# Kernel optimization log

Measured on AMD Instinct MI355X. Metric: run time of the kernel, lower is better.

The kernel has to match this reference:

```python
import math
import jax, jax.numpy as jnp
import numpy as np

H = 16  # head_count

def setup_inputs() -> dict:
    key = jax.random.key(0)
    ks = jax.random.split(key, 7)
    B, S, D = 2, 2048, 1024
    query = jax.random.normal(ks[0], (B, S, D), dtype=jnp.float32)
    # mask: True = masked position (matches masked_fill_ semantics)
    mask = jax.random.randint(ks[1], (B, S, S), 0, 2) > 0
    scale = 1.0 / math.sqrt(D)  # xavier-ish init scale
    Wq = jax.random.normal(ks[2], (D, D), dtype=jnp.float32) * scale
    Wk = jax.random.normal(ks[3], (D, D), dtype=jnp.float32) * scale
    Wv = jax.random.normal(ks[4], (D, D), dtype=jnp.float32) * scale
    Wo = jax.random.normal(ks[5], (D, D), dtype=jnp.float32) * scale
    bo = jnp.zeros((D,), dtype=jnp.float32)
    return {"query": query, "mask": mask, "Wq": Wq, "Wk": Wk, "Wv": Wv, "Wo": Wo, "bo": bo}


def reference(query, mask, Wq, Wk, Wv, Wo, bo):
    B, S, D = query.shape
    dh = D // H

    def split_heads(x):  # [B,S,D] -> [B,H,S,dh]
        return x.reshape(B, S, H, dh).transpose(0, 2, 1, 3)

    # torch nn.Linear computes x @ W.T (bias-free for q/k/v)
    q = split_heads(query @ Wq.T) * (1.0 / math.sqrt(dh))
    k = split_heads(query @ Wk.T)
    v = split_heads(query @ Wv.T)

    scores = jnp.einsum('bhqd,bhkd->bhqk', q, k)           # [B,H,S,S]
    scores = jnp.where(mask[:, None, :, :], jnp.float32(-1e18), scores)
    weights = jax.nn.softmax(scores, axis=-1)               # dropout=0 -> identity
    ctx = jnp.einsum('bhqk,bhkd->bhqd', weights, v)         # [B,H,S,dh]
    ctx = ctx.transpose(0, 2, 1, 3).reshape(B, S, D)        # combine heads
    return ctx @ Wo.T + bo
```

## Files before the change

### kernel.cpp

```cpp
#include <hip/hip_runtime.h>

#define S_LEN 2048
#define D_MODEL 1024
#define NH 16
#define DH 64

typedef __bf16 bf16x8 __attribute__((ext_vector_type(8)));
typedef __bf16 bf16x4 __attribute__((ext_vector_type(4)));
typedef float f32x4 __attribute__((ext_vector_type(4)));

__device__ __forceinline__ unsigned short f2bf(float f) {
  unsigned int x = __float_as_uint(f);
  x += 0x7fffu + ((x >> 16) & 1u);
  return (unsigned short)(x >> 16);
}

__device__ __forceinline__ bf16x4 cvt4(f32x4 v) {
  return __builtin_convertvector(v, bf16x4);
}

__device__ __forceinline__ float exp2raw(float x) {
#if __has_builtin(__builtin_amdgcn_exp2f)
  return __builtin_amdgcn_exp2f(x);
#else
  return exp2f(x);
#endif
}

__device__ __forceinline__ f32x4 mfma16(bf16x8 a, bf16x8 b, f32x4 c) {
  return __builtin_amdgcn_mfma_f32_16x16x32_bf16(a, b, c, 0, 0, 0);
}

__device__ __forceinline__ void gl2lds(const unsigned short* g, unsigned short* l) {
  __builtin_amdgcn_global_load_lds(
      (__attribute__((address_space(1))) void*)g,
      (__attribute__((address_space(3))) void*)l, 16, 0, 0);
}

__global__ __launch_bounds__(256) void prep_kernel(
    const float* __restrict__ q, const float* __restrict__ wq,
    const float* __restrict__ wk, const float* __restrict__ wv,
    const float* __restrict__ wo, const int* __restrict__ mask,
    unsigned short* __restrict__ qbf, unsigned short* __restrict__ wbf,
    unsigned long long* __restrict__ bits) {
  const int bx = blockIdx.x;
  if (bx < 32768) {
    int i = bx * 256 + threadIdx.x;
    unsigned long long bal = __ballot(mask[i] != 0);
    if ((threadIdx.x & 63) == 0) bits[i >> 6] = bal;
  } else {
    const long t = (long)(bx - 32768) * 256 + threadIdx.x;
    const float* src;
    unsigned short* dst;
    long e;
    if (t < 524288) { src = q; dst = qbf; e = t * 8; }
    else {
      long u = t - 524288;
      int wi = (int)(u >> 17);
      e = (u & 131071) * 8;
      src = wi == 0 ? wq : wi == 1 ? wk : wi == 2 ? wv : wo;
      dst = wbf + (long)wi * 1048576;
    }
    float4 a = *(const float4*)(src + e);
    float4 b = *(const float4*)(src + e + 4);
    ushort4 p0 = {f2bf(a.x), f2bf(a.y), f2bf(a.z), f2bf(a.w)};
    ushort4 p1 = {f2bf(b.x), f2bf(b.y), f2bf(b.z), f2bf(b.w)};
    *(ushort4*)(dst + e) = p0;
    *(ushort4*)(dst + e + 4) = p1;
  }
}

__global__ __launch_bounds__(256) void gemm_qkv(
    const unsigned short* __restrict__ A, const unsigned short* __restrict__ W3,
    unsigned short* __restrict__ qb, unsigned short* __restrict__ kb,
    unsigned short* __restrict__ vt, float qscale) {
  __shared__ unsigned short As[128 * 64];
  __shared__ unsigned short Bs[128 * 64];
  const int tid = threadIdx.x, lane = tid & 63, wid = tid >> 6;
  const int wm = wid >> 1, wn = wid & 1;
  const int quad = lane >> 4, c = lane & 15, cx = c & 7;
  const int nG = blockIdx.x * 128;
  const int wi = nG >> 10, nn0 = nG & 1023;
  const int m0 = blockIdx.y * 128;
  const unsigned short* Bsrc = W3 + (size_t)wi * 1048576;
  const int srow = lane >> 3;
  const int schk = ((lane & 7) ^ srow) * 8;
  const unsigned short* ag = A + (size_t)(m0 + wid * 32 + srow) * 1024 + schk;
  const unsigned short* bg = Bsrc + (size_t)(nn0 + wid * 32 + srow) * 1024 + schk;
  f32x4 acc[4][4] = {};
  for (int kk = 0; kk < 1024; kk += 64) {
#pragma unroll
    for (int i = 0; i < 4; ++i) {
      gl2lds(ag + (size_t)(i * 8) * 1024 + kk, &As[(wid * 32 + i * 8) * 64]);
      gl2lds(bg + (size_t)(i * 8) * 1024 + kk, &Bs[(wid * 32 + i * 8) * 64]);
    }
    __syncthreads();
#pragma unroll
    for (int kc = 0; kc < 2; ++kc) {
      bf16x8 a[4], b[4];
#pragma unroll
      for (int mt = 0; mt < 4; ++mt)
        a[mt] = *(const bf16x8*)(
            &As[(wm * 64 + mt * 16 + c) * 64 + ((kc * 4 + quad) ^ cx) * 8]);
#pragma unroll
      for (int nt = 0; nt < 4; ++nt)
        b[nt] = *(const bf16x8*)(
            &Bs[(wn * 64 + nt * 16 + c) * 64 + ((kc * 4 + quad) ^ cx) * 8]);
#pragma unroll
      for (int mt = 0; mt < 4; ++mt)
#pragma unroll
        for (int nt = 0; nt < 4; ++nt)
          acc[mt][nt] = mfma16(a[mt], b[nt], acc[mt][nt]);
    }
    __syncthreads();
  }
#pragma unroll
  for (int mt = 0; mt < 4; ++mt) {
#pragma unroll
    for (int nt = 0; nt < 4; ++nt) {
      const int mb = m0 + wm * 64 + mt * 16 + quad * 4;
      const int n = nn0 + wn * 64 + nt * 16 + c;
      const int hh = n >> 6, d = n & 63;
      const int bb = mb >> 11, ss = mb & 2047;
      if (wi == 0) {
#pragma unroll
        for (int r = 0; r < 4; ++r)
          qb[(size_t)((bb * NH + hh) * S_LEN + ss + r) * DH + d] =
              f2bf(acc[mt][nt][r] * qscale);
      } else if (wi == 1) {
#pragma unroll
        for (int r = 0; r < 4; ++r)
          kb[(size_t)((bb * NH + hh) * S_LEN + ss + r) * DH + d] =
              f2bf(acc[mt][nt][r]);
      } else {
        *(bf16x4*)(vt + (size_t)((bb * NH + hh) * DH + d) * S_LEN + ss) =
            cvt4(acc[mt][nt]);
      }
    }
  }
}

__global__ __launch_bounds__(256) void gemm_out(
    const unsigned short* __restrict__ A, const unsigned short* __restrict__ W,
    float* __restrict__ out, const float* __restrict__ bias) {
  __shared__ unsigned short As[128 * 64];
  __shared__ unsigned short Bs[64 * 64];
  const int tid = threadIdx.x, lane = tid & 63, wid = tid >> 6;
  const int wm = wid >> 1, wn = wid & 1;
  const int quad = lane >> 4, c = lane & 15, cx = c & 7;
  const int n0 = blockIdx.x * 64, m0 = blockIdx.y * 128;
  const int srow = lane >> 3;
  const int schk = ((lane & 7) ^ srow) * 8;
  const unsigned short* ag = A + (size_t)(m0 + wid * 32 + srow) * 1024 + schk;
  const unsigned short* bg = W + (size_t)(n0 + wid * 16 + srow) * 1024 + schk;
  f32x4 acc[4][2] = {};
  for (int kk = 0; kk < 1024; kk += 64) {
#pragma unroll
    for (int i = 0; i < 4; ++i)
      gl2lds(ag + (size_t)(i * 8) * 1024 + kk, &As[(wid * 32 + i * 8) * 64]);
#pragma unroll
    for (int i = 0; i < 2; ++i)
      gl2lds(bg + (size_t)(i * 8) * 1024 + kk, &Bs[(wid * 16 + i * 8) * 64]);
    __syncthreads();
#pragma unroll
    for (int kc = 0; kc < 2; ++kc) {
      bf16x8 a[4], b[2];
#pragma unroll
      for (int mt = 0; mt < 4; ++mt)
        a[mt] = *(const bf16x8*)(
            &As[(wm * 64 + mt * 16 + c) * 64 + ((kc * 4 + quad) ^ cx) * 8]);
#pragma unroll
      for (int nt = 0; nt < 2; ++nt)
        b[nt] = *(const bf16x8*)(
            &Bs[(wn * 32 + nt * 16 + c) * 64 + ((kc * 4 + quad) ^ cx) * 8]);
#pragma unroll
      for (int mt = 0; mt < 4; ++mt)
#pragma unroll
        for (int nt = 0; nt < 2; ++nt)
          acc[mt][nt] = mfma16(a[mt], b[nt], acc[mt][nt]);
    }
    __syncthreads();
  }
#pragma unroll
  for (int mt = 0; mt < 4; ++mt) {
#pragma unroll
    for (int nt = 0; nt < 2; ++nt) {
      const int mb = m0 + wm * 64 + mt * 16 + quad * 4;
      const int n = n0 + wn * 32 + nt * 16 + c;
      const float bv = bias[n];
#pragma unroll
      for (int r = 0; r < 4; ++r)
        out[(size_t)(mb + r) * D_MODEL + n] = acc[mt][nt][r] + bv;
    }
  }
}

__global__ __launch_bounds__(256, 2) void attn_kernel(
    const unsigned short* __restrict__ qb, const unsigned short* __restrict__ kb,
    const unsigned short* __restrict__ vt,
    const unsigned long long* __restrict__ mbits,
    unsigned short* __restrict__ ctx) {
  const int h = blockIdx.x, qt = blockIdx.y, b = blockIdx.z;
  const int bh = b * NH + h;
  const int tid = threadIdx.x, lane = tid & 63, wid = tid >> 6;
  const int quad = lane >> 4, c = lane & 15, cx = c & 7;
  const int qw = wid & 1, kh = wid >> 1;
  const int q0 = qt * 128;
  __shared__ __align__(16) char smem[35328];
  unsigned short* KVb = (unsigned short*)smem;

  const int qbase = q0 + qw * 64;
  const unsigned short* qp = qb + (size_t)(bh * S_LEN + qbase + c) * DH;
  bf16x8 bq[4][2];
#pragma unroll
  for (int sub = 0; sub < 4; ++sub) {
    bq[sub][0] = *(const bf16x8*)(qp + sub * 16 * DH + quad * 8);
    bq[sub][1] = *(const bf16x8*)(qp + sub * 16 * DH + 32 + quad * 8);
  }

  f32x4 o[4][4] = {};
  float lacc[4] = {0.f, 0.f, 0.f, 0.f};
  const unsigned long long* mq0 =
      mbits + (size_t)(b * S_LEN + qbase + c) * 32 + kh * 16;

  const int srow = lane >> 3, schk = ((lane & 7) ^ srow) * 8;
  const unsigned short* Ksh = KVb + kh * 4096;
  const unsigned short* Vsh = KVb + (2 + kh) * 4096;

  const unsigned short* gKb =
      kb + (size_t)(bh * S_LEN + (wid & 1) * 1024) * DH + schk;
  const unsigned short* gV =
      vt + (size_t)(bh * DH + srow) * S_LEN + (wid - 2) * 1024 + schk;

  for (int kt = 0; kt < 1024; kt += 64) {
    if (wid < 2) {
#pragma unroll
      for (int i = 0; i < 8; ++i) {
        const int t = i * 8 + srow;
        const int st = (t & 0x23) | ((t >> 2) & 0x04) | ((t << 1) & 0x18);
        gl2lds(gKb + (size_t)(kt + st) * DH, &KVb[wid * 4096 + i * 512]);
      }
    } else {
#pragma unroll
      for (int i = 0; i < 8; ++i)
        gl2lds(gV + (size_t)(i * 8) * S_LEN + kt, &KVb[wid * 4096 + i * 512]);
    }
    __syncthreads();

    bf16x8 kf[8];
#pragma unroll
    for (int g = 0; g < 4; ++g) {
      const int rho = g * 16 + c;
      kf[2 * g] = *(const bf16x8*)(&Ksh[rho * 64 + (quad ^ cx) * 8]);
      kf[2 * g + 1] = *(const bf16x8*)(&Ksh[rho * 64 + ((4 + quad) ^ cx) * 8]);
    }

    const int mi = kt >> 6;
    bf16x8 bps[4][2];
#pragma unroll
    for (int sub = 0; sub < 4; ++sub) {
      f32x4 s[4];
#pragma unroll
      for (int g = 0; g < 4; ++g) {
        f32x4 z = {};
        z = mfma16(kf[2 * g], bq[sub][0], z);
        z = mfma16(kf[2 * g + 1], bq[sub][1], z);
        s[g] = z;
      }
      const unsigned long long w64 = mq0[sub * 512 + mi];
      const unsigned int wlo = (unsigned int)w64;
      const unsigned int whi = (unsigned int)(w64 >> 32);
      float lp = 0.f;
      f32x4 p[4];
#pragma unroll
      for (int g = 0; g < 4; ++g) {
        const unsigned int bits =
            ((g & 2) ? whi : wlo) >> (quad * 8 + (g & 1) * 4);
#pragma unroll
        for (int r = 0; r < 4; ++r) {
          const float e = exp2raw(s[g][r]);
          p[g][r] = ((bits >> r) & 1u) ? 0.f : e;
          lp += p[g][r];
        }
      }
      union { bf16x8 v; bf16x4 h[2]; } u0, u1;
      u0.h[0] = cvt4(p[0]); u0.h[1] = cvt4(p[1]);
      u1.h[0] = cvt4(p[2]); u1.h[1] = cvt4(p[3]);
      bps[sub][0] = u0.v;
      bps[sub][1] = u1.v;
      lacc[sub] += lp;
    }

#pragma unroll
    for (int ks = 0; ks < 2; ++ks) {
#pragma unroll
      for (int nt = 0; nt < 4; ++nt) {
        bf16x8 av = *(const bf16x8*)(
            &Vsh[(nt * 16 + c) * 64 + ((ks * 4 + quad) ^ cx) * 8]);
#pragma unroll
        for (int sub = 0; sub < 4; ++sub)
          o[sub][nt] = mfma16(av, bps[sub][ks], o[sub][nt]);
      }
    }
    __syncthreads();
  }

#pragma unroll
  for (int sub = 0; sub < 4; ++sub) {
    lacc[sub] += __shfl_xor(lacc[sub], 16, 64);
    lacc[sub] += __shfl_xor(lacc[sub], 32, 64);
  }

  float* mrg = (float*)smem;
  float* ml = mrg + 8 * 1088;
  if (kh == 1) {
#pragma unroll
    for (int sub = 0; sub < 4; ++sub) {
      float* mo = mrg + (qw * 4 + sub) * 1088;
#pragma unroll
      for (int nt = 0; nt < 4; ++nt)
        *(f32x4*)(mo + c * 68 + nt * 16 + quad * 4) = o[sub][nt];
      if (quad == 0) ml[(qw * 4 + sub) * 16 + c] = lacc[sub];
    }
  }
  __syncthreads();
  if (kh == 0) {
#pragma unroll
    for (int sub = 0; sub < 4; ++sub) {
      const int pp = qw * 4 + sub;
      const float inv = 1.0f / (lacc[sub] + ml[pp * 16 + c]);
      const int q = qbase + sub * 16 + c;
      const float* mo = mrg + pp * 1088;
#pragma unroll
      for (int nt = 0; nt < 4; ++nt) {
        f32x4 ob = *(const f32x4*)(mo + c * 68 + nt * 16 + quad * 4);
        f32x4 rr = (o[sub][nt] + ob) * inv;
        *(bf16x4*)(ctx + (size_t)(b * S_LEN + q) * D_MODEL + h * DH + nt * 16 +
                   quad * 4) = cvt4(rr);
      }
    }
  }
}

extern "C" void kernel_launch(void* const* d_in, const int* in_sizes, int n_in,
                              void* d_out, int out_size, void* d_ws, size_t ws_size,
                              hipStream_t stream) {
  const float* query = (const float*)d_in[0];
  const int* mask = (const int*)d_in[1];
  const float* Wq = (const float*)d_in[2];
  const float* Wk = (const float*)d_in[3];
  const float* Wv = (const float*)d_in[4];
  const float* Wo = (const float*)d_in[5];
  const float* bo = (const float*)d_in[6];
  float* out = (float*)d_out;

  char* ws = (char*)d_ws;
  const size_t MB = 1024 * 1024;
  unsigned short* qbf = (unsigned short*)(ws);
  unsigned short* wbf = (unsigned short*)(ws + 8 * MB);
  unsigned short* qb = (unsigned short*)(ws + 16 * MB);
  unsigned short* kb = (unsigned short*)(ws + 24 * MB);
  unsigned short* vt = (unsigned short*)(ws + 32 * MB);
  unsigned long long* mb = (unsigned long long*)(ws + 40 * MB);
  unsigned short* ctx = qbf;

  prep_kernel<<<32768 + 4096, 256, 0, stream>>>(query, Wq, Wk, Wv, Wo, mask,
                                                qbf, wbf, mb);

  gemm_qkv<<<dim3(3072 / 128, 4096 / 128), 256, 0, stream>>>(
      qbf, wbf, qb, kb, vt, 0.18033688f);

  attn_kernel<<<dim3(NH, S_LEN / 128, 2), 256, 0, stream>>>(qb, kb, vt, mb,
                                                            ctx);

  gemm_out<<<dim3(1024 / 64, 4096 / 128), 256, 0, stream>>>(
      ctx, wbf + 3 * 1048576, out, bo);
}
```

Measured before the change: 222.0 us.

## Split attention key range across four wave groups with 512-thread blocks

The attention kernel grows from 256 to 512 threads. Each pair of query waves now covers a quarter of the key sequence instead of a half, and K and V tiles get separate LDS regions sized for four key slices. The partial outputs and softmax denominators from the four slices are combined through shared memory in several synchronized steps. The aim is to shorten each block's serial key loop and put more waves per SIMD to hide latency. In exchange it uses more LDS, adds merge synchronization, and tightens the register budget through the new launch bounds, which risks spilling.

```diff
diff --git a/kernel.cpp b/kernel.cpp
--- a/kernel.cpp
+++ b/kernel.cpp
@@ -195,7 +195,7 @@
   }
 }
 
-__global__ __launch_bounds__(256, 2) void attn_kernel(
+__global__ __launch_bounds__(512, 4) void attn_kernel(
     const unsigned short* __restrict__ qb, const unsigned short* __restrict__ kb,
     const unsigned short* __restrict__ vt,
     const unsigned long long* __restrict__ mbits,
@@ -204,9 +204,9 @@
   const int bh = b * NH + h;
   const int tid = threadIdx.x, lane = tid & 63, wid = tid >> 6;
   const int quad = lane >> 4, c = lane & 15, cx = c & 7;
-  const int qw = wid & 1, kh = wid >> 1;
+  const int qw = wid & 1, kq = wid >> 1;
   const int q0 = qt * 128;
-  __shared__ __align__(16) char smem[35328];
+  __shared__ __align__(16) char smem[65536];
   unsigned short* KVb = (unsigned short*)smem;
 
   const int qbase = q0 + qw * 64;
@@ -221,29 +221,29 @@
   f32x4 o[4][4] = {};
   float lacc[4] = {0.f, 0.f, 0.f, 0.f};
   const unsigned long long* mq0 =
-      mbits + (size_t)(b * S_LEN + qbase + c) * 32 + kh * 16;
+      mbits + (size_t)(b * S_LEN + qbase + c) * 32 + kq * 8;
 
   const int srow = lane >> 3, schk = ((lane & 7) ^ srow) * 8;
-  const unsigned short* Ksh = KVb + kh * 4096;
-  const unsigned short* Vsh = KVb + (2 + kh) * 4096;
+  unsigned short* Ksh = KVb + kq * 4096;
+  unsigned short* Vsh = KVb + 16384 + kq * 4096;
 
   const unsigned short* gKb =
-      kb + (size_t)(bh * S_LEN + (wid & 1) * 1024) * DH + schk;
+      kb + (size_t)(bh * S_LEN + kq * 512) * DH + schk;
   const unsigned short* gV =
-      vt + (size_t)(bh * DH + srow) * S_LEN + (wid - 2) * 1024 + schk;
-
-  for (int kt = 0; kt < 1024; kt += 64) {
-    if (wid < 2) {
+      vt + (size_t)(bh * DH + srow) * S_LEN + kq * 512 + schk;
+
+  for (int kt = 0; kt < 512; kt += 64) {
+    if (qw == 0) {
 #pragma unroll
       for (int i = 0; i < 8; ++i) {
         const int t = i * 8 + srow;
         const int st = (t & 0x23) | ((t >> 2) & 0x04) | ((t << 1) & 0x18);
-        gl2lds(gKb + (size_t)(kt + st) * DH, &KVb[wid * 4096 + i * 512]);
+        gl2lds(gKb + (size_t)(kt + st) * DH, &Ksh[i * 512]);
       }
     } else {
 #pragma unroll
       for (int i = 0; i < 8; ++i)
-        gl2lds(gV + (size_t)(i * 8) * S_LEN + kt, &KVb[wid * 4096 + i * 512]);
+        gl2lds(gV + (size_t)(i * 8) * S_LEN + kt, &Vsh[i * 512]);
     }
     __syncthreads();
 
@@ -313,7 +313,7 @@
 
   float* mrg = (float*)smem;
   float* ml = mrg + 8 * 1088;
-  if (kh == 1) {
+  if (kq == 1) {
 #pragma unroll
     for (int sub = 0; sub < 4; ++sub) {
       float* mo = mrg + (qw * 4 + sub) * 1088;
@@ -324,7 +324,51 @@
     }
   }
   __syncthreads();
-  if (kh == 0) {
+  if (kq == 0) {
+#pragma unroll
+    for (int sub = 0; sub < 4; ++sub) {
+      const float* mo = mrg + (qw * 4 + sub) * 1088;
+#pragma unroll
+      for (int nt = 0; nt < 4; ++nt)
+        o[sub][nt] += *(const f32x4*)(mo + c * 68 + nt * 16 + quad * 4);
+      lacc[sub] += ml[(qw * 4 + sub) * 16 + c];
+    }
+  }
+  __syncthreads();
+  if (kq == 3) {
+#pragma unroll
+    for (int sub = 0; sub < 4; ++sub) {
+      float* mo = mrg + (qw * 4 + sub) * 1088;
+#pragma unroll
+      for (int nt = 0; nt < 4; ++nt)
+        *(f32x4*)(mo + c * 68 + nt * 16 + quad * 4) = o[sub][nt];
+      if (quad == 0) ml[(qw * 4 + sub) * 16 + c] = lacc[sub];
+    }
+  }
+  __syncthreads();
+  if (kq == 2) {
+#pragma unroll
+    for (int sub = 0; sub < 4; ++sub) {
+      const float* mo = mrg + (qw * 4 + sub) * 1088;
+#pragma unroll
+      for (int nt = 0; nt < 4; ++nt)
+        o[sub][nt] += *(const f32x4*)(mo + c * 68 + nt * 16 + quad * 4);
+      lacc[sub] += ml[(qw * 4 + sub) * 16 + c];
+    }
+  }
+  __syncthreads();
+  if (kq == 2) {
+#pragma unroll
+    for (int sub = 0; sub < 4; ++sub) {
+      float* mo = mrg + (qw * 4 + sub) * 1088;
+#pragma unroll
+      for (int nt = 0; nt < 4; ++nt)
+        *(f32x4*)(mo + c * 68 + nt * 16 + quad * 4) = o[sub][nt];
+      if (quad == 0) ml[(qw * 4 + sub) * 16 + c] = lacc[sub];
+    }
+  }
+  __syncthreads();
+  if (kq == 0) {
 #pragma unroll
     for (int sub = 0; sub < 4; ++sub) {
       const int pp = qw * 4 + sub;
@@ -370,7 +414,7 @@
   gemm_qkv<<<dim3(3072 / 128, 4096 / 128), 256, 0, stream>>>(
       qbf, wbf, qb, kb, vt, 0.18033688f);
 
-  attn_kernel<<<dim3(NH, S_LEN / 128, 2), 256, 0, stream>>>(qb, kb, vt, mb,
+  attn_kernel<<<dim3(NH, S_LEN / 128, 2), 512, 0, stream>>>(qb, kb, vt, mb,
                                                             ctx);
 
   gemm_out<<<dim3(1024 / 64, 4096 / 128), 256, 0, stream>>>(
```

After: 381.2 us. 1.72x slower.

## Double-buffer K/V tiles in LDS to overlap loads with attention compute

Applied to the files above, without the earlier changes.

Grows the attention kernel's shared memory to two 32 KB K/V stages and prefetches the next 64-key tile while the current one is being used for QK^T, masking, exp and PV MFMAs. This drops one barrier per iteration and hides global-to-LDS latency. It also reorganises the row-sum accumulation into a vector tree reduction. The cost is much higher LDS usage (64 KB per block), which may lower occupancy below the two blocks per CU requested by launch_bounds.

```diff
diff --git a/kernel.cpp b/kernel.cpp
--- a/kernel.cpp
+++ b/kernel.cpp
@@ -206,7 +206,7 @@
   const int quad = lane >> 4, c = lane & 15, cx = c & 7;
   const int qw = wid & 1, kh = wid >> 1;
   const int q0 = qt * 128;
-  __shared__ __align__(16) char smem[35328];
+  __shared__ __align__(16) char smem[65536];
   unsigned short* KVb = (unsigned short*)smem;
 
   const int qbase = q0 + qw * 64;
@@ -224,28 +224,36 @@
       mbits + (size_t)(b * S_LEN + qbase + c) * 32 + kh * 16;
 
   const int srow = lane >> 3, schk = ((lane & 7) ^ srow) * 8;
-  const unsigned short* Ksh = KVb + kh * 4096;
-  const unsigned short* Vsh = KVb + (2 + kh) * 4096;
 
   const unsigned short* gKb =
       kb + (size_t)(bh * S_LEN + (wid & 1) * 1024) * DH + schk;
   const unsigned short* gV =
       vt + (size_t)(bh * DH + srow) * S_LEN + (wid - 2) * 1024 + schk;
 
-  for (int kt = 0; kt < 1024; kt += 64) {
-    if (wid < 2) {
-#pragma unroll
-      for (int i = 0; i < 8; ++i) {
-        const int t = i * 8 + srow;
-        const int st = (t & 0x23) | ((t >> 2) & 0x04) | ((t << 1) & 0x18);
-        gl2lds(gKb + (size_t)(kt + st) * DH, &KVb[wid * 4096 + i * 512]);
-      }
-    } else {
-#pragma unroll
-      for (int i = 0; i < 8; ++i)
-        gl2lds(gV + (size_t)(i * 8) * S_LEN + kt, &KVb[wid * 4096 + i * 512]);
-    }
-    __syncthreads();
+#define STAGE(buf, kt)                                                        \
+  do {                                                                        \
+    unsigned short* dst = KVb + (buf)*16384 + wid * 4096;                     \
+    if (wid < 2) {                                                            \
+      _Pragma("unroll") for (int i = 0; i < 8; ++i) {                         \
+        const int t = i * 8 + srow;                                           \
+        const int st = (t & 0x23) | ((t >> 2) & 0x04) | ((t << 1) & 0x18);    \
+        gl2lds(gKb + (size_t)((kt) + st) * DH, &dst[i * 512]);                \
+      }                                                                       \
+    } else {                                                                  \
+      _Pragma("unroll") for (int i = 0; i < 8; ++i)                           \
+          gl2lds(gV + (size_t)(i * 8) * S_LEN + (kt), &dst[i * 512]);         \
+    }                                                                         \
+  } while (0)
+
+  STAGE(0, 0);
+  __syncthreads();
+
+  for (int it = 0; it < 16; ++it) {
+    const int cur = it & 1;
+    if (it < 15) STAGE(cur ^ 1, (it + 1) * 64);
+
+    const unsigned short* Ksh = KVb + cur * 16384 + kh * 4096;
+    const unsigned short* Vsh = KVb + cur * 16384 + (2 + kh) * 4096;
 
     bf16x8 kf[8];
 #pragma unroll
@@ -255,7 +263,6 @@
       kf[2 * g + 1] = *(const bf16x8*)(&Ksh[rho * 64 + ((4 + quad) ^ cx) * 8]);
     }
 
-    const int mi = kt >> 6;
     bf16x8 bps[4][2];
 #pragma unroll
     for (int sub = 0; sub < 4; ++sub) {
@@ -267,10 +274,9 @@
         z = mfma16(kf[2 * g + 1], bq[sub][1], z);
         s[g] = z;
       }
-      const unsigned long long w64 = mq0[sub * 512 + mi];
+      const unsigned long long w64 = mq0[sub * 512 + it];
       const unsigned int wlo = (unsigned int)w64;
       const unsigned int whi = (unsigned int)(w64 >> 32);
-      float lp = 0.f;
       f32x4 p[4];
 #pragma unroll
       for (int g = 0; g < 4; ++g) {
@@ -280,15 +286,17 @@
         for (int r = 0; r < 4; ++r) {
           const float e = exp2raw(s[g][r]);
           p[g][r] = ((bits >> r) & 1u) ? 0.f : e;
-          lp += p[g][r];
         }
       }
+      f32x4 t01 = p[0] + p[1];
+      f32x4 t23 = p[2] + p[3];
+      f32x4 ts = t01 + t23;
+      lacc[sub] += (ts[0] + ts[1]) + (ts[2] + ts[3]);
       union { bf16x8 v; bf16x4 h[2]; } u0, u1;
       u0.h[0] = cvt4(p[0]); u0.h[1] = cvt4(p[1]);
       u1.h[0] = cvt4(p[2]); u1.h[1] = cvt4(p[3]);
       bps[sub][0] = u0.v;
       bps[sub][1] = u1.v;
-      lacc[sub] += lp;
     }
 
 #pragma unroll
@@ -304,6 +312,7 @@
     }
     __syncthreads();
   }
+#undef STAGE
 
 #pragma unroll
   for (int sub = 0; sub < 4; ++sub) {
```

New measurement: 224.6 us. About the same (+1.1%).

## Load 128-key K/V tiles per sync and compute row sums with MFMA

Applied to the files above, without the earlier changes.

The attention loop now stages two 64-key K/V halves in shared memory per iteration, which halves the number of barriers and lets more global-to-LDS traffic be in flight at once. Shared memory grows to 64 KB per block, which may limit occupancy under launch_bounds(256,2). The softmax denominator is now accumulated with an MFMA against a ones vector on the bf16-rounded probabilities instead of scalar adds and cross-lane shuffles. This moves the row-sum work onto the matrix unit and keeps it consistent with the bf16 P used in the PV product.

```diff
diff --git a/kernel.cpp b/kernel.cpp
--- a/kernel.cpp
+++ b/kernel.cpp
@@ -206,7 +206,7 @@
   const int quad = lane >> 4, c = lane & 15, cx = c & 7;
   const int qw = wid & 1, kh = wid >> 1;
   const int q0 = qt * 128;
-  __shared__ __align__(16) char smem[35328];
+  __shared__ __align__(16) char smem[65536];
   unsigned short* KVb = (unsigned short*)smem;
 
   const int qbase = q0 + qw * 64;
@@ -217,6 +217,9 @@
     bq[sub][0] = *(const bf16x8*)(qp + sub * 16 * DH + quad * 8);
     bq[sub][1] = *(const bf16x8*)(qp + sub * 16 * DH + 32 + quad * 8);
   }
+
+  const bf16x8 onesv = {(__bf16)1.f, (__bf16)1.f, (__bf16)1.f, (__bf16)1.f,
+                        (__bf16)1.f, (__bf16)1.f, (__bf16)1.f, (__bf16)1.f};
 
   f32x4 o[4][4] = {};
   float lacc[4] = {0.f, 0.f, 0.f, 0.f};
@@ -224,91 +227,97 @@
       mbits + (size_t)(b * S_LEN + qbase + c) * 32 + kh * 16;
 
   const int srow = lane >> 3, schk = ((lane & 7) ^ srow) * 8;
-  const unsigned short* Ksh = KVb + kh * 4096;
-  const unsigned short* Vsh = KVb + (2 + kh) * 4096;
 
   const unsigned short* gKb =
       kb + (size_t)(bh * S_LEN + (wid & 1) * 1024) * DH + schk;
   const unsigned short* gV =
       vt + (size_t)(bh * DH + srow) * S_LEN + (wid - 2) * 1024 + schk;
 
-  for (int kt = 0; kt < 1024; kt += 64) {
+  for (int kt = 0; kt < 1024; kt += 128) {
     if (wid < 2) {
 #pragma unroll
-      for (int i = 0; i < 8; ++i) {
-        const int t = i * 8 + srow;
-        const int st = (t & 0x23) | ((t >> 2) & 0x04) | ((t << 1) & 0x18);
-        gl2lds(gKb + (size_t)(kt + st) * DH, &KVb[wid * 4096 + i * 512]);
-      }
+      for (int hf = 0; hf < 2; ++hf)
+#pragma unroll
+        for (int i = 0; i < 8; ++i) {
+          const int t = i * 8 + srow;
+          const int st = (t & 0x23) | ((t >> 2) & 0x04) | ((t << 1) & 0x18);
+          gl2lds(gKb + (size_t)(kt + hf * 64 + st) * DH,
+                 &KVb[hf * 16384 + wid * 4096 + i * 512]);
+        }
     } else {
 #pragma unroll
-      for (int i = 0; i < 8; ++i)
-        gl2lds(gV + (size_t)(i * 8) * S_LEN + kt, &KVb[wid * 4096 + i * 512]);
-    }
-    __syncthreads();
-
-    bf16x8 kf[8];
-#pragma unroll
-    for (int g = 0; g < 4; ++g) {
-      const int rho = g * 16 + c;
-      kf[2 * g] = *(const bf16x8*)(&Ksh[rho * 64 + (quad ^ cx) * 8]);
-      kf[2 * g + 1] = *(const bf16x8*)(&Ksh[rho * 64 + ((4 + quad) ^ cx) * 8]);
-    }
-
-    const int mi = kt >> 6;
-    bf16x8 bps[4][2];
-#pragma unroll
-    for (int sub = 0; sub < 4; ++sub) {
-      f32x4 s[4];
+      for (int hf = 0; hf < 2; ++hf)
+#pragma unroll
+        for (int i = 0; i < 8; ++i)
+          gl2lds(gV + (size_t)(i * 8) * S_LEN + kt + hf * 64,
+                 &KVb[hf * 16384 + wid * 4096 + i * 512]);
+    }
+    __syncthreads();
+
+#pragma unroll
+    for (int hf = 0; hf < 2; ++hf) {
+      const unsigned short* Ksh = KVb + hf * 16384 + kh * 4096;
+      const unsigned short* Vsh = KVb + hf * 16384 + (2 + kh) * 4096;
+      const int mi = (kt >> 6) + hf;
+
+      bf16x8 kf[8];
 #pragma unroll
       for (int g = 0; g < 4; ++g) {
-        f32x4 z = {};
-        z = mfma16(kf[2 * g], bq[sub][0], z);
-        z = mfma16(kf[2 * g + 1], bq[sub][1], z);
-        s[g] = z;
-      }
-      const unsigned long long w64 = mq0[sub * 512 + mi];
-      const unsigned int wlo = (unsigned int)w64;
-      const unsigned int whi = (unsigned int)(w64 >> 32);
-      float lp = 0.f;
-      f32x4 p[4];
-#pragma unroll
-      for (int g = 0; g < 4; ++g) {
-        const unsigned int bits =
-            ((g & 2) ? whi : wlo) >> (quad * 8 + (g & 1) * 4);
-#pragma unroll
-        for (int r = 0; r < 4; ++r) {
-          const float e = exp2raw(s[g][r]);
-          p[g][r] = ((bits >> r) & 1u) ? 0.f : e;
-          lp += p[g][r];
+        const int rho = g * 16 + c;
+        kf[2 * g] = *(const bf16x8*)(&Ksh[rho * 64 + (quad ^ cx) * 8]);
+        kf[2 * g + 1] =
+            *(const bf16x8*)(&Ksh[rho * 64 + ((4 + quad) ^ cx) * 8]);
+      }
+
+      bf16x8 bps[4][2];
+#pragma unroll
+      for (int sub = 0; sub < 4; ++sub) {
+        f32x4 s[4];
+#pragma unroll
+        for (int g = 0; g < 4; ++g) {
+          f32x4 z = {};
+          z = mfma16(kf[2 * g], bq[sub][0], z);
+          z = mfma16(kf[2 * g + 1], bq[sub][1], z);
+          s[g] = z;
         }
-      }
-      union { bf16x8 v; bf16x4 h[2]; } u0, u1;
-      u0.h[0] = cvt4(p[0]); u0.h[1] = cvt4(p[1]);
-      u1.h[0] = cvt4(p[2]); u1.h[1] = cvt4(p[3]);
-      bps[sub][0] = u0.v;
-      bps[sub][1] = u1.v;
-      lacc[sub] += lp;
-    }
-
-#pragma unroll
-    for (int ks = 0; ks < 2; ++ks) {
-#pragma unroll
-      for (int nt = 0; nt < 4; ++nt) {
-        bf16x8 av = *(const bf16x8*)(
-            &Vsh[(nt * 16 + c) * 64 + ((ks * 4 + quad) ^ cx) * 8]);
-#pragma unroll
-        for (int sub = 0; sub < 4; ++sub)
-          o[sub][nt] = mfma16(av, bps[sub][ks], o[sub][nt]);
-      }
-    }
-    __syncthreads();
-  }
-
-#pragma unroll
-  for (int sub = 0; sub < 4; ++sub) {
-    lacc[sub] += __shfl_xor(lacc[sub], 16, 64);
-    lacc[sub] += __shfl_xor(lacc[sub], 32, 64);
+        const unsigned long long w64 = mq0[sub * 512 + mi];
+        const unsigned int wlo = (unsigned int)w64;
+        const unsigned int whi = (unsigned int)(w64 >> 32);
+        f32x4 p[4];
+#pragma unroll
+        for (int g = 0; g < 4; ++g) {
+          const unsigned int bits =
+              ((g & 2) ? whi : wlo) >> (quad * 8 + (g & 1) * 4);
+#pragma unroll
+          for (int r = 0; r < 4; ++r) {
+            const float e = exp2raw(s[g][r]);
+            p[g][r] = ((bits >> r) & 1u) ? 0.f : e;
+          }
+        }
+        union { bf16x8 v; bf16x4 h[2]; } u0, u1;
+        u0.h[0] = cvt4(p[0]); u0.h[1] = cvt4(p[1]);
+        u1.h[0] = cvt4(p[2]); u1.h[1] = cvt4(p[3]);
+        bps[sub][0] = u0.v;
+        bps[sub][1] = u1.v;
+        f32x4 zs = {};
+        zs = mfma16(onesv, bps[sub][0], zs);
+        zs = mfma16(onesv, bps[sub][1], zs);
+        lacc[sub] += zs[0];
+      }
+
+#pragma unroll
+      for (int ks = 0; ks < 2; ++ks) {
+#pragma unroll
+        for (int nt = 0; nt < 4; ++nt) {
+          bf16x8 av = *(const bf16x8*)(
+              &Vsh[(nt * 16 + c) * 64 + ((ks * 4 + quad) ^ cx) * 8]);
+#pragma unroll
+          for (int sub = 0; sub < 4; ++sub)
+            o[sub][nt] = mfma16(av, bps[sub][ks], o[sub][nt]);
+        }
+      }
+    }
+    __syncthreads();
   }
 
   float* mrg = (float*)smem;
```

Result: no change. 221.1 us (-0.4%).
